# Kernel optimization log

Measured on AMD Instinct MI355X. Metric: run time of the kernel, lower is better.

The kernel has to match this reference:

```python
import jax, jax.numpy as jnp
import numpy as np

L, H, D_MODEL, FFN = 2, 8, 1024, 4096
HD = D_MODEL // H          # head size = 128
SCALE_BASE = 512           # XPOS scale_base
EPS = 1e-5                 # LayerNorm / GroupNorm eps (torch default)


def _layernorm(x, w, b):
    mu = x.mean(-1, keepdims=True)
    var = ((x - mu) ** 2).mean(-1, keepdims=True)
    return (x - mu) * jax.lax.rsqrt(var + EPS) * w + b


def _groupnorm(y, w, b):
    # GroupNorm(heads, v_dim) applied row-wise on (B*S, v_dim): normalize each head's HD slice.
    B, S, _ = y.shape
    yg = y.reshape(B, S, H, HD)
    mu = yg.mean(-1, keepdims=True)
    var = ((yg - mu) ** 2).mean(-1, keepdims=True)
    yn = ((yg - mu) * jax.lax.rsqrt(var + EPS)).reshape(B, S, H * HD)
    return yn * w + b


def _xpos_tables(S):
    # XPOS: scale = ((arange(0,HD,2)+0.4*HD)/(1.4*HD)) ** (pos/scale_base); sin/cos from fixed_pos_embedding(scale)
    scale_vec = (np.arange(0, HD, 2) + 0.4 * HD) / (1.4 * HD)            # (HD/2,)
    power = (np.arange(S, dtype=np.float64) / SCALE_BASE)[:, None]
    scale = scale_vec[None, :] ** power                                   # (S, HD/2)
    half = HD // 2
    inv_freq = 1.0 / (10000.0 ** (np.arange(half, dtype=np.float64) / half))
    ang = np.arange(S, dtype=np.float64)[:, None] * inv_freq[None, :]
    sin, cos = np.sin(ang), np.cos(ang)
    dup = lambda m: jnp.asarray(np.repeat(m, 2, axis=-1).astype(np.float32))  # duplicate_interleave -> (S, HD)
    return dup(sin * scale), dup(cos * scale), dup(sin / scale), dup(cos / scale)


def _rotate_every_two(x):
    x1, x2 = x[..., ::2], x[..., 1::2]
    return jnp.stack((-x2, x1), axis=-1).reshape(x.shape)


def _decay_mask(S):
    # gammas = 1 - exp(linspace(log(1/32), log(1/512), H)); D[h,n,m] = gamma_h^(n-m) * (n>=m)
    gammas = 1.0 - np.exp(np.linspace(np.log(1.0 / 32), np.log(1.0 / 512), H))
    n = np.arange(S)[:, None]
    m = np.arange(S)[None, :]
    diff = (n - m).astype(np.float64)
    D = np.where(n >= m, gammas[:, None, None] ** diff[None], 0.0)
    return jnp.asarray(D.astype(np.float32))  # (H, S, S)


def setup_inputs() -> dict:
    key = jax.random.key(0)
    ks = jax.random.split(key, 8)
    B, S = 2, 2048
    rn = lambda k, shape, s: jax.random.normal(k, shape, dtype=jnp.float32) * s
    return {
        "X": rn(ks[0], (B, S, D_MODEL), 1.0),
        "ln1_w": jnp.ones((L, D_MODEL), jnp.float32), "ln1_b": jnp.zeros((L, D_MODEL), jnp.float32),
        "ln2_w": jnp.ones((L, D_MODEL), jnp.float32), "ln2_b": jnp.zeros((L, D_MODEL), jnp.float32),
        "WQ": rn(ks[1], (L, H, D_MODEL, HD), 1.0 / D_MODEL),
        "WK": rn(ks[2], (L, H, D_MODEL, HD), 1.0 / D_MODEL),
        "WV": rn(ks[3], (L, H, D_MODEL, HD), 1.0 / D_MODEL),
        "gn_w": jnp.ones((L, D_MODEL), jnp.float32), "gn_b": jnp.zeros((L, D_MODEL), jnp.float32),
        "WG": rn(ks[4], (L, D_MODEL, D_MODEL), 1.0 / D_MODEL),
        "WO": rn(ks[5], (L, D_MODEL, D_MODEL), 1.0 / D_MODEL),
        "ffn_w1": rn(ks[6], (L, D_MODEL, FFN), 1.0 / np.sqrt(D_MODEL)),
        "ffn_b1": jnp.zeros((L, FFN), jnp.float32),
        "ffn_w2": rn(ks[7], (L, FFN, D_MODEL), 1.0 / np.sqrt(FFN)),
        "ffn_b2": jnp.zeros((L, D_MODEL), jnp.float32),
    }


def reference(X, ln1_w, ln1_b, ln2_w, ln2_b, WQ, WK, WV, gn_w, gn_b, WG, WO,
              ffn_w1, ffn_b1, ffn_w2, ffn_b2):
    B, S, _ = X.shape
    sinq, cosq, sink, cosk = _xpos_tables(S)   # (S, HD) each; K uses downscale (1/scale)
    Dm = _decay_mask(S)                         # (H, S, S)
    for i in range(L):
        Xn = _layernorm(X, ln1_w[i], ln1_b[i])
        Q = jnp.einsum('bsd,hdk->bhsk', Xn, WQ[i])
        K = jnp.einsum('bsd,hdk->bhsk', Xn, WK[i])
        V = jnp.einsum('bsd,hdk->bhsk', Xn, WV[i])
        Q = Q * cosq + _rotate_every_two(Q) * sinq
        K = K * cosk + _rotate_every_two(K) * sink
        scores = jnp.einsum('bhsk,bhtk->bhst', Q, K) * Dm[None]  # decay-masked retention
        Yh = jnp.einsum('bhst,bhtk->bhsk', scores, V)
        Y = Yh.transpose(0, 2, 1, 3).reshape(B, S, H * HD)        # concat heads
        Y = _groupnorm(Y, gn_w[i], gn_b[i])
        G = jax.nn.silu(Xn @ WG[i])                               # swish gate on layernormed input
        Y = (G * Y) @ WO[i] + X                                   # retention + residual
        Yn = _layernorm(Y, ln2_w[i], ln2_b[i])
        X = jax.nn.silu(Yn @ ffn_w1[i] + ffn_b1[i]) @ ffn_w2[i] + ffn_b2[i] + Y
    return X
```

## Files before the change

kernel.cpp:

```cpp
#include <hip/hip_runtime.h>
#include <cstdint>
#include <cstddef>

#define LN_ 2
#define HH 8
#define DM 1024
#define FFN_ 4096
#define HDD 128
#define SS 2048
#define BB 2
#define RR (BB*SS)

typedef __bf16 bf16x8 __attribute__((ext_vector_type(8)));
typedef __bf16 bf16x4 __attribute__((ext_vector_type(4)));
typedef __bf16 bf16x2 __attribute__((ext_vector_type(2)));
typedef float  f32x4  __attribute__((ext_vector_type(4)));

__device__ __forceinline__ float silu_f(float x) { return x / (1.0f + expf(-x)); }

__device__ __forceinline__ void glds16(const void* g, void* l) {
  __builtin_amdgcn_global_load_lds(
      (const __attribute__((address_space(1))) unsigned int*)g,
      (__attribute__((address_space(3))) unsigned int*)l, 16, 0, 0);
}


__device__ __forceinline__ int xcd_swz(int lin, int nblk) {
  return (lin & 7) * (nblk >> 3) + (lin >> 3);
}

__global__ void init_tables_k(float* __restrict__ sq, float* __restrict__ cq,
                              float* __restrict__ sk, float* __restrict__ ck,
                              float* __restrict__ lg2g) {
  int s = blockIdx.x, k = threadIdx.x;
  int j = k >> 1;
  double sv    = (2.0 * j + 0.4 * HDD) / (1.4 * HDD);
  double p     = (double)s / 512.0;
  double scale = pow(sv, p);
  double invf  = pow(10000.0, -((double)j) / 64.0);
  double ang   = (double)s * invf;
  double sn = sin(ang), cs = cos(ang);
  size_t idx = (size_t)s * HDD + k;
  sq[idx] = (float)(sn * scale);
  cq[idx] = (float)(cs * scale);
  sk[idx] = (float)(sn / scale);
  ck[idx] = (float)(cs / scale);
  if (s == 0 && k < HH) {
    double a0 = log(1.0 / 32.0), a1 = log(1.0 / 512.0);
    double x = a0 + (a1 - a0) * ((double)k / 7.0);
    lg2g[k] = (float)(log(1.0 - exp(x)) / log(2.0));
  }
}

__global__ __launch_bounds__(256) void ln_pack_k(
    const float* __restrict__ X, const float* __restrict__ w,
    const float* __restrict__ b, char* __restrict__ ph, char* __restrict__ pl) {
  const int row = blockIdx.x, tid = threadIdx.x;
  const float* x = X + (size_t)row * DM;
  float4 v = *(const float4*)(x + tid * 4);
  float s = v.x + v.y + v.z + v.w;
  float q = v.x * v.x + v.y * v.y + v.z * v.z + v.w * v.w;
#pragma unroll
  for (int o = 32; o > 0; o >>= 1) { s += __shfl_xor(s, o); q += __shfl_xor(q, o); }
  __shared__ float ss[4], qq[4];
  if ((tid & 63) == 0) { ss[tid >> 6] = s; qq[tid >> 6] = q; }
  __syncthreads();
  float S  = ss[0] + ss[1] + ss[2] + ss[3];
  float Qs = qq[0] + qq[1] + qq[2] + qq[3];
  float mu  = S * (1.0f / DM);
  float var = Qs * (1.0f / DM) - mu * mu;
  float rs  = 1.0f / sqrtf(var + 1e-5f);
  float4 wv = *(const float4*)(w + tid * 4);
  float4 bv = *(const float4*)(b + tid * 4);
  float y[4];
  y[0] = (v.x - mu) * rs * wv.x + bv.x;
  y[1] = (v.y - mu) * rs * wv.y + bv.y;
  y[2] = (v.z - mu) * rs * wv.z + bv.z;
  y[3] = (v.w - mu) * rs * wv.w + bv.w;
  bf16x4 hv, lv;
#pragma unroll
  for (int r = 0; r < 4; ++r) {
    __bf16 h = (__bf16)y[r];
    hv[r] = h;
    lv[r] = (__bf16)(y[r] - (float)h);
  }
  size_t tb = ((size_t)(row >> 7) * (DM / 64) + (tid >> 4)) * 16384;
  int off = (row & 127) * 128 + (((tid & 15) * 8) ^ ((row & 7) << 4));
  *(bf16x4*)(ph + tb + off) = hv;
  *(bf16x4*)(pl + tb + off) = lv;
}

__global__ __launch_bounds__(256) void packw_k(
    const float* __restrict__ W, char* __restrict__ dh, char* __restrict__ dl,
    int N, int qkv) {
  const int tn = blockIdx.x, tk = blockIdx.y, nkt = gridDim.y;
  __shared__ float L[64][132];
  const int k0 = tk * 64;
  const size_t srcbase = qkv ? ((size_t)tn * 131072 + (size_t)k0 * 128)
                             : ((size_t)k0 * N + (size_t)tn * 128);
  const int rstr = qkv ? 128 : N;
#pragma unroll
  for (int it = 0; it < 8; ++it) {
    int q = threadIdx.x + it * 256;
    int kk = q >> 5, c4 = (q & 31) * 4;
    float4 v = *(const float4*)(W + srcbase + (size_t)kk * rstr + c4);
    *(float4*)&L[kk][c4] = v;
  }
  __syncthreads();
  const size_t tb = ((size_t)tn * nkt + tk) * 16384;
#pragma unroll
  for (int it = 0; it < 4; ++it) {
    int o = threadIdx.x + it * 256;
    int n = o >> 3, k8 = o & 7;
    bf16x8 hv, lv;
#pragma unroll
    for (int j = 0; j < 8; ++j) {
      float x = L[k8 * 8 + j][n];
      __bf16 h = (__bf16)x;
      hv[j] = h;
      lv[j] = (__bf16)(x - (float)h);
    }
    int off = n * 128 + ((k8 * 16) ^ ((n & 7) << 4));
    *(bf16x8*)(dh + tb + off) = hv;
    *(bf16x8*)(dl + tb + off) = lv;
  }
}

__global__ __launch_bounds__(256) void vtpack_k(
    const float* __restrict__ V, char* __restrict__ dh, char* __restrict__ dl) {
  const int st = blockIdx.x, bh = blockIdx.y;
  __shared__ float L[64][132];
  const float* src = V + ((size_t)bh * SS + st * 64) * HDD;
#pragma unroll
  for (int it = 0; it < 8; ++it) {
    int q = threadIdx.x + it * 256;
    int r = q >> 5, c4 = (q & 31) * 4;
    *(float4*)&L[r][c4] = *(const float4*)(src + (size_t)r * HDD + c4);
  }
  __syncthreads();
  const size_t tb = ((size_t)bh * 32 + st) * 16384;
#pragma unroll
  for (int it = 0; it < 4; ++it) {
    int o = threadIdx.x + it * 256;
    int d = o >> 3, s8 = o & 7;
    bf16x8 hv, lv;
#pragma unroll
    for (int j = 0; j < 8; ++j) {
      float x = L[s8 * 8 + j][d];
      __bf16 h = (__bf16)x;
      hv[j] = h;
      lv[j] = (__bf16)(x - (float)h);
    }
    int off = d * 128 + ((s8 * 16) ^ ((d & 7) << 4));
    *(bf16x8*)(dh + tb + off) = hv;
    *(bf16x8*)(dl + tb + off) = lv;
  }
}

template <int NF>
__device__ __forceinline__ void gemm_main(
    const char* __restrict__ pAh, const char* __restrict__ pAl,
    const char* __restrict__ pBh, const char* __restrict__ pBl,
    size_t tA0, size_t tB0, int nkt, char* lds, f32x4 (&acc)[NF][4]) {
  const int tid = threadIdx.x, lane = tid & 63, w = tid >> 6;
  const int wm = w & 1, wn = w >> 1;
  const int swz = (lane & 7) << 4;
  const int l15 = lane & 15, l4 = lane >> 4;
  char* lAh = lds;
  char* lAl = lds + 16384;
  char* lBh = lds + 32768;
  char* lBl = lds + 32768 + NF * 4096;
  for (int t = 0; t < nkt; ++t) {
    const size_t oA = tA0 + (size_t)t * 16384;
    const size_t oB = tB0 + (size_t)t * 16384;
#pragma unroll
    for (int c = 0; c < 4; ++c) {
      const size_t go = (size_t)c * 4096 + w * 1024 + lane * 16;
      glds16(pAh + oA + go, lAh + c * 4096 + w * 1024);
      glds16(pAl + oA + go, lAl + c * 4096 + w * 1024);
    }
#pragma unroll
    for (int c = 0; c < NF; ++c) {
      const size_t go = (size_t)c * 4096 + w * 1024 + lane * 16;
      glds16(pBh + oB + go, lBh + c * 4096 + w * 1024);
      glds16(pBl + oB + go, lBl + c * 4096 + w * 1024);
    }
    __syncthreads();
#pragma unroll
    for (int ks = 0; ks < 2; ++ks) {
      const int kb = ks * 64 + l4 * 16;
      bf16x8 amh[4], aml[4], anh[NF], anl[NF];
#pragma unroll
      for (int f = 0; f < 4; ++f) {
        const int ra = (wm * 64 + f * 16 + l15) * 128 + (kb ^ swz);
        amh[f] = *(const bf16x8*)&lAh[ra];
        aml[f] = *(const bf16x8*)&lAl[ra];
      }
#pragma unroll
      for (int f = 0; f < NF; ++f) {
        const int rb = (wn * (NF * 16) + f * 16 + l15) * 128 + (kb ^ swz);
        anh[f] = *(const bf16x8*)&lBh[rb];
        anl[f] = *(const bf16x8*)&lBl[rb];
      }
#pragma unroll
      for (int nf = 0; nf < NF; ++nf)
#pragma unroll
        for (int mf = 0; mf < 4; ++mf) {
          acc[nf][mf] = __builtin_amdgcn_mfma_f32_16x16x32_bf16(
              anh[nf], amh[mf], acc[nf][mf], 0, 0, 0);
          acc[nf][mf] = __builtin_amdgcn_mfma_f32_16x16x32_bf16(
              anh[nf], aml[mf], acc[nf][mf], 0, 0, 0);
          acc[nf][mf] = __builtin_amdgcn_mfma_f32_16x16x32_bf16(
              anl[nf], amh[mf], acc[nf][mf], 0, 0, 0);
        }
    }
    __syncthreads();
  }
}

template <int MODE, int NF>
__global__ __launch_bounds__(256, (NF == 2 ? 3 : 2)) void mgemm_k(
    const char* __restrict__ pAh, const char* __restrict__ pAl,
    const char* __restrict__ pBh, const char* __restrict__ pBl,
    float* __restrict__ C, const float* __restrict__ bias,
    const float* __restrict__ resid, char* __restrict__ outH,
    char* __restrict__ outL, int N, int K) {
  __shared__ char lds[32768 + NF * 8192];
  const int lane = threadIdx.x & 63, w = threadIdx.x >> 6;
  const int wm = w & 1, wn = w >> 1;
  const int l15 = lane & 15, l4 = lane >> 4;
  const int lin = blockIdx.y * gridDim.x + blockIdx.x;
  const int swzb = xcd_swz(lin, gridDim.x * gridDim.y);
  const int bx = swzb % gridDim.x, by = swzb / gridDim.x;
  const int nkt = K >> 6;
  const size_t tA0 = (size_t)by * nkt * 16384;
  const size_t tB0 = (NF == 4) ? (size_t)bx * nkt * 16384
                               : (size_t)(bx >> 1) * nkt * 16384 + (size_t)(bx & 1) * 8192;
  f32x4 acc[NF][4];
#pragma unroll
  for (int i = 0; i < NF; ++i)
#pragma unroll
    for (int j = 0; j < 4; ++j) acc[i][j] = (f32x4){0.f, 0.f, 0.f, 0.f};

  gemm_main<NF>(pAh, pAl, pBh, pBl, tA0, tB0, nkt, lds, acc);

  const int mBase = by * 128 + wm * 64 + l15;
  const int nBase = bx * (NF * 32) + wn * (NF * 16) + l4 * 4;
#pragma unroll
  for (int nf = 0; nf < NF; ++nf)
#pragma unroll
    for (int mf = 0; mf < 4; ++mf) {
      const int m = mBase + mf * 16;
      const int n = nBase + nf * 16;
      f32x4 v = acc[nf][mf];
      if (MODE == 2) {
        f32x4 rz = *(const f32x4*)(resid + (size_t)m * N + n);
        v += rz;
        *(f32x4*)(C + (size_t)m * N + n) = v;
      } else if (MODE == 3) {
        f32x4 bz = *(const f32x4*)(bias + n);
        bf16x4 hv, lv;
#pragma unroll
        for (int r = 0; r < 4; ++r) {
          float y = silu_f(v[r] + bz[r]);
          __bf16 h = (__bf16)y;
          hv[r] = h;
          lv[r] = (__bf16)(y - (float)h);
        }
        size_t tb = ((size_t)(m >> 7) * (N >> 6) + (n >> 6)) * 16384;
        int off = (m & 127) * 128 + (((n & 63) * 2) ^ ((m & 7) << 4));
        *(bf16x4*)(outH + tb + off) = hv;
        *(bf16x4*)(outL + tb + off) = lv;
      } else {
        f32x4 bz = *(const f32x4*)(bias + n);
        f32x4 rz = *(const f32x4*)(resid + (size_t)m * N + n);
        v += bz + rz;
        *(f32x4*)(C + (size_t)m * N + n) = v;
      }
    }
}

__global__ __launch_bounds__(256, 2) void qkvg_k(
    const char* __restrict__ pXh, const char* __restrict__ pXl,
    const char* __restrict__ pWh, const char* __restrict__ pWl,
    float* __restrict__ V, float* __restrict__ G,
    char* __restrict__ pQh, char* __restrict__ pQl,
    char* __restrict__ pKh, char* __restrict__ pKl,
    const float* __restrict__ sq, const float* __restrict__ cq,
    const float* __restrict__ sk, const float* __restrict__ ck) {
  __shared__ char lds[65536];
  const int lane = threadIdx.x & 63, w = threadIdx.x >> 6;
  const int wm = w & 1, wn = w >> 1;
  const int l15 = lane & 15, l4 = lane >> 4;
  const int lin = ((blockIdx.z * 32) + blockIdx.y) * 8 + blockIdx.x;
  const int swzb = xcd_swz(lin, 1024);
  const int bx = swzb & 7, by = (swzb >> 3) & 31, z = swzb >> 8;
  const int nkt = DM >> 6;
  const size_t tA0 = (size_t)by * nkt * 16384;
  const size_t tB0 = (size_t)bx * nkt * 16384;
  const size_t wo = (size_t)z << 21;
  f32x4 acc[4][4];
#pragma unroll
  for (int i = 0; i < 4; ++i)
#pragma unroll
    for (int j = 0; j < 4; ++j) acc[i][j] = (f32x4){0.f, 0.f, 0.f, 0.f};

  gemm_main<4>(pXh, pXl, pWh + wo, pWl + wo, tA0, tB0, nkt, lds, acc);

  const int mBase = by * 128 + wm * 64 + l15;
  const int nBase = bx * 128 + wn * 64 + l4 * 4;
#pragma unroll
  for (int nf = 0; nf < 4; ++nf)
#pragma unroll
    for (int mf = 0; mf < 4; ++mf) {
      const int m = mBase + mf * 16;
      const int n = nBase + nf * 16;
      f32x4 v = acc[nf][mf];
      if (z == 2) {
        *(f32x4*)(V + (((size_t)(m >> 11) * HH + (n >> 7)) * SS + (m & (SS - 1)))
                          * HDD + (n & (HDD - 1))) = v;
      } else if (z == 3) {
#pragma unroll
        for (int r = 0; r < 4; ++r) v[r] = silu_f(v[r]);
        *(f32x4*)(G + (size_t)m * DM + n) = v;
      } else {
        const float* tsn = (z == 0) ? sq : sk;
        const float* tcs = (z == 0) ? cq : ck;
        char* oh = (z == 0) ? pQh : pKh;
        char* ol = (z == 0) ? pQl : pKl;
        int s = m & (SS - 1);
        int d = n & (HDD - 1);
        f32x4 sn = *(const f32x4*)(tsn + (size_t)s * HDD + d);
        f32x4 cn = *(const f32x4*)(tcs + (size_t)s * HDD + d);
        float o0 = v[0] * cn[0] - v[1] * sn[0];
        float o1 = v[1] * cn[1] + v[0] * sn[1];
        float o2 = v[2] * cn[2] - v[3] * sn[2];
        float o3 = v[3] * cn[3] + v[2] * sn[3];
        float oo[4] = {o0, o1, o2, o3};
        bf16x4 hv, lv;
#pragma unroll
        for (int r = 0; r < 4; ++r) {
          __bf16 h = (__bf16)oo[r];
          hv[r] = h;
          lv[r] = (__bf16)(oo[r] - (float)h);
        }
        size_t tile = ((size_t)(m >> 11) * HH + (n >> 7)) * 32 + (s >> 7) * 2 + (d >> 6);
        size_t off = tile * 16384 + (s & 127) * 128 + (((d & 63) * 2) ^ ((s & 7) << 4));
        *(bf16x4*)(oh + off) = hv;
        *(bf16x4*)(ol + off) = lv;
      }
    }
}

__global__ __launch_bounds__(256, 2) void mattn_k(
    const char* __restrict__ pQh, const char* __restrict__ pQl,
    const char* __restrict__ pKh, const char* __restrict__ pKl,
    const char* __restrict__ pVh, const char* __restrict__ pVl,
    const float* __restrict__ lg2g, float* __restrict__ Y) {
  __shared__ char Kls[2][2][8192];
  __shared__ char Vls[2][16384];
  __shared__ char Pls[2][8192];
  const int lin = blockIdx.y * 32 + blockIdx.x;
  const int swzb = xcd_swz(lin, 512);
  const int qt = 31 - (swzb & 31);
  const int bh = swzb >> 5;
  const int tid = threadIdx.x, lane = tid & 63, w = tid >> 6;
  const int wn = w & 1, wq = w >> 1;
  const int l15 = lane & 15, lg = lane >> 4;
  const float lg2 = lg2g[bh & 7];
  const size_t tb0 = (size_t)bh * 32;
  const int n0 = qt * 64;
  const int nt = qt + 1;

  bf16x8 qh[2][4], ql[2][4];
#pragma unroll
  for (int nf = 0; nf < 2; ++nf) {
    int rr = n0 + wn * 32 + nf * 16 + l15;
    size_t rowbase = (tb0 + (size_t)(rr >> 7) * 2) * 16384 + (size_t)(rr & 127) * 128;
    int sw = (rr & 7) << 4;
#pragma unroll
    for (int ks = 0; ks < 4; ++ks) {
      int d = ks * 32 + lg * 8;
      size_t a = rowbase + (size_t)(d >> 6) * 16384 + (((d & 63) * 2) ^ sw);
      qh[nf][ks] = *(const bf16x8*)(pQh + a);
      ql[nf][ks] = *(const bf16x8*)(pQl + a);
    }
  }

  f32x4 yacc[2][4];
#pragma unroll
  for (int i = 0; i < 2; ++i)
#pragma unroll
    for (int j = 0; j < 4; ++j) yacc[i][j] = (f32x4){0.f, 0.f, 0.f, 0.f};

  auto stageK = [&](int mt) {
    size_t half = (size_t)(mt & 1) * 8192;
#pragma unroll
    for (int dt = 0; dt < 2; ++dt) {
      size_t tile = (tb0 + (size_t)(mt >> 1) * 2 + dt) * 16384 + half;
#pragma unroll
      for (int c = 0; c < 2; ++c) {
        size_t go = (size_t)c * 4096 + w * 1024 + lane * 16;
        glds16(pKh + tile + go, &Kls[dt][0][c * 4096 + w * 1024]);
        glds16(pKl + tile + go, &Kls[dt][1][c * 4096 + w * 1024]);
      }
    }
  };
  auto stageV = [&](int mt) {
    size_t tile = (tb0 + mt) * 16384;
#pragma unroll
    for (int c = 0; c < 4; ++c) {
      size_t go = (size_t)c * 4096 + w * 1024 + lane * 16;
      glds16(pVh + tile + go, &Vls[0][c * 4096 + w * 1024]);
      glds16(pVl + tile + go, &Vls[1][c * 4096 + w * 1024]);
    }
  };

  stageK(0);
  stageV(0);
  __syncthreads();

  for (int mt = 0; mt < nt; ++mt) {
    f32x4 sacc[2][2];
#pragma unroll
    for (int i = 0; i < 2; ++i)
#pragma unroll
      for (int j = 0; j < 2; ++j) sacc[i][j] = (f32x4){0.f, 0.f, 0.f, 0.f};
#pragma unroll
    for (int ks = 0; ks < 4; ++ks) {
      int d = ks * 32 + lg * 8;
      bf16x8 kh[2], kl[2];
#pragma unroll
      for (int mf = 0; mf < 2; ++mf) {
        int m = wq * 32 + mf * 16 + l15;
        int off = (m & 63) * 128 + (((d & 63) * 2) ^ ((m & 7) << 4));
        kh[mf] = *(const bf16x8*)&Kls[d >> 6][0][off];
        kl[mf] = *(const bf16x8*)&Kls[d >> 6][1][off];
      }
#pragma unroll
      for (int nf = 0; nf < 2; ++nf)
#pragma unroll
        for (int mf = 0; mf < 2; ++mf) {
          sacc[nf][mf] = __builtin_amdgcn_mfma_f32_16x16x32_bf16(
              qh[nf][ks], kh[mf], sacc[nf][mf], 0, 0, 0);
          sacc[nf][mf] = __builtin_amdgcn_mfma_f32_16x16x32_bf16(
              qh[nf][ks], kl[mf], sacc[nf][mf], 0, 0, 0);
          sacc[nf][mf] = __builtin_amdgcn_mfma_f32_16x16x32_bf16(
              ql[nf][ks], kh[mf], sacc[nf][mf], 0, 0, 0);
        }
    }
    asm volatile("s_barrier" ::: "memory");
    if (mt + 1 < nt) stageK(mt + 1);

#pragma unroll
    for (int nf = 0; nf < 2; ++nf)
#pragma unroll
      for (int mf = 0; mf < 2; ++mf)
#pragma unroll
        for (int r = 0; r < 4; ++r) {
          int nl = wn * 32 + nf * 16 + lg * 4 + r;
          int ml = wq * 32 + mf * 16 + l15;
          int diff = (n0 + nl) - (mt * 64 + ml);
          float dec = (diff >= 0) ? exp2f((float)diff * lg2) : 0.0f;
          float p = sacc[nf][mf][r] * dec;
          __bf16 h = (__bf16)p;
          int off = nl * 128 + ((ml * 2) ^ ((nl & 7) << 4));
          *(__bf16*)&Pls[0][off] = h;
          *(__bf16*)&Pls[1][off] = (__bf16)(p - (float)h);
        }
    asm volatile("s_waitcnt lgkmcnt(0)" ::: "memory");
    asm volatile("s_barrier" ::: "memory");

#pragma unroll
    for (int ks = 0; ks < 2; ++ks) {
      int mchunk = ks * 32 + lg * 8;
      bf16x8 ph[2], pl2[2], vh[4], vl2[4];
#pragma unroll
      for (int nf = 0; nf < 2; ++nf) {
        int nl = wn * 32 + nf * 16 + l15;
        int off = nl * 128 + ((mchunk * 2) ^ ((nl & 7) << 4));
        ph[nf]  = *(const bf16x8*)&Pls[0][off];
        pl2[nf] = *(const bf16x8*)&Pls[1][off];
      }
#pragma unroll
      for (int df = 0; df < 4; ++df) {
        int d = wq * 64 + df * 16 + l15;
        int off = d * 128 + ((mchunk * 2) ^ ((d & 7) << 4));
        vh[df]  = *(const bf16x8*)&Vls[0][off];
        vl2[df] = *(const bf16x8*)&Vls[1][off];
      }
#pragma unroll
      for (int nf = 0; nf < 2; ++nf)
#pragma unroll
        for (int df = 0; df < 4; ++df) {
          yacc[nf][df] = __builtin_amdgcn_mfma_f32_16x16x32_bf16(
              ph[nf], vh[df], yacc[nf][df], 0, 0, 0);
          yacc[nf][df] = __builtin_amdgcn_mfma_f32_16x16x32_bf16(
              ph[nf], vl2[df], yacc[nf][df], 0, 0, 0);
          yacc[nf][df] = __builtin_amdgcn_mfma_f32_16x16x32_bf16(
              pl2[nf], vh[df], yacc[nf][df], 0, 0, 0);
        }
    }
    asm volatile("s_barrier" ::: "memory");
    if (mt + 1 < nt) stageV(mt + 1);
    __syncthreads();
  }

  const size_t yrow0 = (size_t)(bh >> 3) * SS + n0;
  const int hcol = (bh & 7) * HDD;
#pragma unroll
  for (int nf = 0; nf < 2; ++nf)
#pragma unroll
    for (int df = 0; df < 4; ++df)
#pragma unroll
      for (int r = 0; r < 4; ++r) {
        int nl = wn * 32 + nf * 16 + lg * 4 + r;
        int d  = wq * 64 + df * 16 + l15;
        Y[(yrow0 + nl) * DM + hcol + d] = yacc[nf][df][r];
      }
}

__global__ __launch_bounds__(256) void gn_gate_k(
    const float* __restrict__ Y, const float* __restrict__ w,
    const float* __restrict__ b, const float* __restrict__ G,
    char* __restrict__ ph, char* __restrict__ pl) {
  int g    = blockIdx.x * 4 + (threadIdx.x >> 6);
  int lane = threadIdx.x & 63;
  float2 v = *(const float2*)(Y + (size_t)g * HDD + lane * 2);
  float s = v.x + v.y, q = v.x * v.x + v.y * v.y;
#pragma unroll
  for (int o = 32; o > 0; o >>= 1) { s += __shfl_xor(s, o); q += __shfl_xor(q, o); }
  float mu  = s * (1.0f / HDD);
  float var = q * (1.0f / HDD) - mu * mu;
  float rs  = 1.0f / sqrtf(var + 1e-5f);
  int m   = g >> 3;
  int col = (g & 7) * HDD + lane * 2;
  float2 wv = *(const float2*)(w + col);
  float2 bv = *(const float2*)(b + col);
  float2 gv = *(const float2*)(G + (size_t)g * HDD + lane * 2);
  float ox = ((v.x - mu) * rs * wv.x + bv.x) * gv.x;
  float oy = ((v.y - mu) * rs * wv.y + bv.y) * gv.y;
  __bf16 hx = (__bf16)ox, hy = (__bf16)oy;
  bf16x2 hv, lv;
  hv[0] = hx; hv[1] = hy;
  lv[0] = (__bf16)(ox - (float)hx); lv[1] = (__bf16)(oy - (float)hy);
  size_t tb = ((size_t)(m >> 7) * (DM / 64) + (col >> 6)) * 16384;
  int off = (m & 127) * 128 + (((col & 63) * 2) ^ ((m & 7) << 4));
  *(bf16x2*)(ph + tb + off) = hv;
  *(bf16x2*)(pl + tb + off) = lv;
}

extern "C" void kernel_launch(void* const* d_in, const int* in_sizes, int n_in,
                              void* d_out, int out_size, void* d_ws, size_t ws_size,
                              hipStream_t stream) {
  (void)in_sizes; (void)n_in; (void)out_size; (void)ws_size;
  const float* X0   = (const float*)d_in[0];
  const float* ln1w = (const float*)d_in[1];
  const float* ln1b = (const float*)d_in[2];
  const float* ln2w = (const float*)d_in[3];
  const float* ln2b = (const float*)d_in[4];
  const float* WQ   = (const float*)d_in[5];
  const float* WK   = (const float*)d_in[6];
  const float* WV   = (const float*)d_in[7];
  const float* gnw  = (const float*)d_in[8];
  const float* gnb  = (const float*)d_in[9];
  const float* WG   = (const float*)d_in[10];
  const float* WO   = (const float*)d_in[11];
  const float* W1   = (const float*)d_in[12];
  const float* B1   = (const float*)d_in[13];
  const float* W2   = (const float*)d_in[14];
  const float* B2   = (const float*)d_in[15];

  char* wsb = (char*)d_ws;
  const size_t MB = 1 << 20;
  float* bufA = (float*)(wsb + 0 * MB);
  float* bufB = (float*)(wsb + 16 * MB);
  float* bufE = (float*)(wsb + 32 * MB);
  float* bufF = (float*)(wsb + 48 * MB);
  float* bufG = (float*)(wsb + 64 * MB);
  float* sq   = (float*)(wsb + 80 * MB);
  float* cq   = (float*)(wsb + 81 * MB);
  float* sk   = (float*)(wsb + 82 * MB);
  float* ck   = (float*)(wsb + 83 * MB);
  float* lg2g = (float*)(wsb + 84 * MB);
  char* pXh = wsb + 85 * MB;
  char* pXl = wsb + 93 * MB;
  char* pWh = wsb + 101 * MB;
  char* pWl = wsb + 127 * MB;
  char* R   = wsb + 153 * MB;
  char* pFh = R;
  char* pFl = R + 32 * MB;
  char* pQh = R;
  char* pQl = R + 8 * MB;
  char* pKh = R + 16 * MB;
  char* pKl = R + 24 * MB;
  char* pVh = R + 32 * MB;
  char* pVl = R + 40 * MB;
  const size_t oWQ = 0, oW1 = (size_t)10 << 20, oWO = (size_t)8 << 20,
               oW2 = (size_t)18 << 20;

  init_tables_k<<<SS, HDD, 0, stream>>>(sq, cq, sk, ck, lg2g);

  for (int i = 0; i < LN_; ++i) {
    const float* Xin = (i == 0) ? X0 : bufA;
    packw_k<<<dim3(8, 16), 256, 0, stream>>>(WQ + (size_t)i * 1048576, pWh + oWQ, pWl + oWQ, 1024, 1);
    packw_k<<<dim3(8, 16), 256, 0, stream>>>(WK + (size_t)i * 1048576, pWh + 2 * MB, pWl + 2 * MB, 1024, 1);
    packw_k<<<dim3(8, 16), 256, 0, stream>>>(WV + (size_t)i * 1048576, pWh + 4 * MB, pWl + 4 * MB, 1024, 1);
    packw_k<<<dim3(8, 16), 256, 0, stream>>>(WG + (size_t)i * 1048576, pWh + 6 * MB, pWl + 6 * MB, 1024, 0);
    packw_k<<<dim3(8, 16), 256, 0, stream>>>(WO + (size_t)i * 1048576, pWh + oWO, pWl + oWO, 1024, 0);
    packw_k<<<dim3(32, 16), 256, 0, stream>>>(W1 + (size_t)i * 4194304, pWh + oW1, pWl + oW1, 4096, 0);
    packw_k<<<dim3(8, 64), 256, 0, stream>>>(W2 + (size_t)i * 4194304, pWh + oW2, pWl + oW2, 1024, 0);

    ln_pack_k<<<RR, 256, 0, stream>>>(Xin, ln1w + i * DM, ln1b + i * DM, pXh, pXl);
    qkvg_k<<<dim3(8, 32, 4), 256, 0, stream>>>(pXh, pXl, pWh, pWl, bufE, bufF,
                                               pQh, pQl, pKh, pKl, sq, cq, sk, ck);
    vtpack_k<<<dim3(32, 16), 256, 0, stream>>>(bufE, pVh, pVl);
    mattn_k<<<dim3(32, 16), 256, 0, stream>>>(pQh, pQl, pKh, pKl, pVh, pVl, lg2g, bufG);
    gn_gate_k<<<RR * HH / 4, 256, 0, stream>>>(bufG, gnw + i * DM, gnb + i * DM,
                                               bufF, pXh, pXl);
    mgemm_k<2, 2><<<dim3(16, 32), 256, 0, stream>>>(pXh, pXl, pWh + oWO, pWl + oWO,
                                                    bufB, nullptr, Xin, nullptr, nullptr,
                                                    DM, DM);
    ln_pack_k<<<RR, 256, 0, stream>>>(bufB, ln2w + i * DM, ln2b + i * DM, pXh, pXl);
    mgemm_k<3, 4><<<dim3(32, 32), 256, 0, stream>>>(pXh, pXl, pWh + oW1, pWl + oW1,
                                                    nullptr, B1 + (size_t)i * FFN_,
                                                    nullptr, pFh, pFl, FFN_, DM);
    float* Xout = (i == LN_ - 1) ? (float*)d_out : bufA;
    mgemm_k<4, 2><<<dim3(16, 32), 256, 0, stream>>>(pFh, pFl, pWh + oW2, pWl + oW2,
                                                    Xout, B2 + (size_t)i * DM, bufB,
                                                    nullptr, nullptr, DM, FFN_);
  }
}
```

Baseline: 1.105 ms.

## Use 8-wave double-buffered GEMM mainloop for QKVG and FFN1 kernels

Adds a new 512-thread (8-wave) GEMM mainloop that double-buffers 128-wide K-steps in 128KB of LDS, issuing async global-to-LDS prefetches two tiles ahead and raising wave priority around the MFMA block. The QKVG projection and the FFN up-projection are switched to this mainloop with each wave owning a 64x32 output sub-tile, and the FFN1 epilogue moves into a dedicated kernel. The aim is to hide global load latency and raise MFMA utilisation through more waves and deeper prefetch. In exchange it uses much more LDS per block, which limits occupancy, and depends on hand-placed waitcnt and barrier ordering being correct.

```diff
diff --git a/kernel.cpp b/kernel.cpp
--- a/kernel.cpp
+++ b/kernel.cpp
@@ -218,13 +218,89 @@
   }
 }
 
+__device__ __forceinline__ void gemm8_main(
+    const char* __restrict__ pAh, const char* __restrict__ pAl,
+    const char* __restrict__ pBh, const char* __restrict__ pBl,
+    size_t tA0, size_t tB0, int nkt, char* lds, f32x4 (&acc)[2][4]) {
+  const int tid = threadIdx.x, lane = tid & 63, wid = tid >> 6;
+  const int wm = wid & 1, wn = wid >> 1;
+  const int l15 = lane & 15, l4 = lane >> 4;
+
+  auto stage = [&](int buf, int t) {
+    const size_t oA = tA0 + (size_t)t * 16384;
+    const size_t oB = tB0 + (size_t)t * 16384;
+    char* lb = lds + buf * 65536;
+#pragma unroll
+    for (int c = 0; c < 2; ++c) {
+      const size_t go = (size_t)c * 8192 + wid * 1024 + lane * 16;
+      const int lo = c * 8192 + wid * 1024;
+      glds16(pAh + oA + go, lb + lo);
+      glds16(pAl + oA + go, lb + 16384 + lo);
+      glds16(pBh + oB + go, lb + 32768 + lo);
+      glds16(pBl + oB + go, lb + 49152 + lo);
+    }
+  };
+
+  auto tile_comp = [&](int buf, bool pf, int pft) {
+    char* lb = lds + buf * 65536;
+    bf16x8 amh[2][4], aml[2][4], bnh[2][2], bnl[2][2];
+#pragma unroll
+    for (int ks = 0; ks < 2; ++ks) {
+      const int kb = ks * 64 + l4 * 16;
+#pragma unroll
+      for (int mf = 0; mf < 4; ++mf) {
+        const int rm = wm * 64 + mf * 16 + l15;
+        const int ra = rm * 128 + (kb ^ ((rm & 7) << 4));
+        amh[ks][mf] = *(const bf16x8*)(lb + ra);
+        aml[ks][mf] = *(const bf16x8*)(lb + 16384 + ra);
+      }
+#pragma unroll
+      for (int nf = 0; nf < 2; ++nf) {
+        const int rn = wn * 32 + nf * 16 + l15;
+        const int rb = rn * 128 + (kb ^ ((rn & 7) << 4));
+        bnh[ks][nf] = *(const bf16x8*)(lb + 32768 + rb);
+        bnl[ks][nf] = *(const bf16x8*)(lb + 49152 + rb);
+      }
+    }
+    asm volatile("s_waitcnt lgkmcnt(0)" ::: "memory");
+    asm volatile("s_barrier" ::: "memory");
+    if (pf) stage(buf, pft);
+    __builtin_amdgcn_s_setprio(1);
+#pragma unroll
+    for (int ks = 0; ks < 2; ++ks)
+#pragma unroll
+      for (int nf = 0; nf < 2; ++nf)
+#pragma unroll
+        for (int mf = 0; mf < 4; ++mf) {
+          acc[nf][mf] = __builtin_amdgcn_mfma_f32_16x16x32_bf16(
+              bnh[ks][nf], amh[ks][mf], acc[nf][mf], 0, 0, 0);
+          acc[nf][mf] = __builtin_amdgcn_mfma_f32_16x16x32_bf16(
+              bnh[ks][nf], aml[ks][mf], acc[nf][mf], 0, 0, 0);
+          acc[nf][mf] = __builtin_amdgcn_mfma_f32_16x16x32_bf16(
+              bnl[ks][nf], amh[ks][mf], acc[nf][mf], 0, 0, 0);
+        }
+    __builtin_amdgcn_s_setprio(0);
+  };
+
+  stage(0, 0);
+  asm volatile("" ::: "memory");
+  stage(1, 1);
+  for (int t = 0; t < nkt - 1; ++t) {
+    asm volatile("s_waitcnt vmcnt(8)" ::: "memory");
+    asm volatile("s_barrier" ::: "memory");
+    tile_comp(t & 1, t + 2 < nkt, t + 2);
+  }
+  asm volatile("s_waitcnt vmcnt(0)" ::: "memory");
+  asm volatile("s_barrier" ::: "memory");
+  tile_comp((nkt - 1) & 1, false, 0);
+}
+
 template <int MODE, int NF>
-__global__ __launch_bounds__(256, (NF == 2 ? 3 : 2)) void mgemm_k(
+__global__ __launch_bounds__(256, 3) void mgemm_k(
     const char* __restrict__ pAh, const char* __restrict__ pAl,
     const char* __restrict__ pBh, const char* __restrict__ pBl,
     float* __restrict__ C, const float* __restrict__ bias,
-    const float* __restrict__ resid, char* __restrict__ outH,
-    char* __restrict__ outL, int N, int K) {
+    const float* __restrict__ resid, int N, int K) {
   __shared__ char lds[32768 + NF * 8192];
   const int lane = threadIdx.x & 63, w = threadIdx.x >> 6;
   const int wm = w & 1, wn = w >> 1;
@@ -234,8 +310,7 @@
   const int bx = swzb % gridDim.x, by = swzb / gridDim.x;
   const int nkt = K >> 6;
   const size_t tA0 = (size_t)by * nkt * 16384;
-  const size_t tB0 = (NF == 4) ? (size_t)bx * nkt * 16384
-                               : (size_t)(bx >> 1) * nkt * 16384 + (size_t)(bx & 1) * 8192;
+  const size_t tB0 = (size_t)(bx >> 1) * nkt * 16384 + (size_t)(bx & 1) * 8192;
   f32x4 acc[NF][4];
 #pragma unroll
   for (int i = 0; i < NF; ++i)
@@ -257,20 +332,6 @@
         f32x4 rz = *(const f32x4*)(resid + (size_t)m * N + n);
         v += rz;
         *(f32x4*)(C + (size_t)m * N + n) = v;
-      } else if (MODE == 3) {
-        f32x4 bz = *(const f32x4*)(bias + n);
-        bf16x4 hv, lv;
-#pragma unroll
-        for (int r = 0; r < 4; ++r) {
-          float y = silu_f(v[r] + bz[r]);
-          __bf16 h = (__bf16)y;
-          hv[r] = h;
-          lv[r] = (__bf16)(y - (float)h);
-        }
-        size_t tb = ((size_t)(m >> 7) * (N >> 6) + (n >> 6)) * 16384;
-        int off = (m & 127) * 128 + (((n & 63) * 2) ^ ((m & 7) << 4));
-        *(bf16x4*)(outH + tb + off) = hv;
-        *(bf16x4*)(outL + tb + off) = lv;
       } else {
         f32x4 bz = *(const f32x4*)(bias + n);
         f32x4 rz = *(const f32x4*)(resid + (size_t)m * N + n);
@@ -280,7 +341,7 @@
     }
 }
 
-__global__ __launch_bounds__(256, 2) void qkvg_k(
+__global__ __launch_bounds__(512, 2) void qkvg8_k(
     const char* __restrict__ pXh, const char* __restrict__ pXl,
     const char* __restrict__ pWh, const char* __restrict__ pWl,
     float* __restrict__ V, float* __restrict__ G,
@@ -288,9 +349,9 @@
     char* __restrict__ pKh, char* __restrict__ pKl,
     const float* __restrict__ sq, const float* __restrict__ cq,
     const float* __restrict__ sk, const float* __restrict__ ck) {
-  __shared__ char lds[65536];
-  const int lane = threadIdx.x & 63, w = threadIdx.x >> 6;
-  const int wm = w & 1, wn = w >> 1;
+  __shared__ char lds[131072];
+  const int lane = threadIdx.x & 63, wid = threadIdx.x >> 6;
+  const int wm = wid & 1, wn = wid >> 1;
   const int l15 = lane & 15, l4 = lane >> 4;
   const int lin = ((blockIdx.z * 32) + blockIdx.y) * 8 + blockIdx.x;
   const int swzb = xcd_swz(lin, 1024);
@@ -299,18 +360,18 @@
   const size_t tA0 = (size_t)by * nkt * 16384;
   const size_t tB0 = (size_t)bx * nkt * 16384;
   const size_t wo = (size_t)z << 21;
-  f32x4 acc[4][4];
-#pragma unroll
-  for (int i = 0; i < 4; ++i)
+  f32x4 acc[2][4];
+#pragma unroll
+  for (int i = 0; i < 2; ++i)
 #pragma unroll
     for (int j = 0; j < 4; ++j) acc[i][j] = (f32x4){0.f, 0.f, 0.f, 0.f};
 
-  gemm_main<4>(pXh, pXl, pWh + wo, pWl + wo, tA0, tB0, nkt, lds, acc);
+  gemm8_main(pXh, pXl, pWh + wo, pWl + wo, tA0, tB0, nkt, lds, acc);
 
   const int mBase = by * 128 + wm * 64 + l15;
-  const int nBase = bx * 128 + wn * 64 + l4 * 4;
-#pragma unroll
-  for (int nf = 0; nf < 4; ++nf)
+  const int nBase = bx * 128 + wn * 32 + l4 * 4;
+#pragma unroll
+  for (int nf = 0; nf < 2; ++nf)
 #pragma unroll
     for (int mf = 0; mf < 4; ++mf) {
       const int m = mBase + mf * 16;
@@ -349,6 +410,55 @@
         *(bf16x4*)(oh + off) = hv;
         *(bf16x4*)(ol + off) = lv;
       }
+    }
+}
+
+__global__ __launch_bounds__(512, 2) void ffn1_8k(
+    const char* __restrict__ pAh, const char* __restrict__ pAl,
+    const char* __restrict__ pBh, const char* __restrict__ pBl,
+    const float* __restrict__ bias, char* __restrict__ outH,
+    char* __restrict__ outL) {
+  __shared__ char lds[131072];
+  const int lane = threadIdx.x & 63, wid = threadIdx.x >> 6;
+  const int wm = wid & 1, wn = wid >> 1;
+  const int l15 = lane & 15, l4 = lane >> 4;
+  const int lin = blockIdx.y * gridDim.x + blockIdx.x;
+  const int swzb = xcd_swz(lin, gridDim.x * gridDim.y);
+  const int bx = swzb % gridDim.x, by = swzb / gridDim.x;
+  const int nkt = DM >> 6;
+  const size_t tA0 = (size_t)by * nkt * 16384;
+  const size_t tB0 = (size_t)bx * nkt * 16384;
+  const int N = FFN_;
+  f32x4 acc[2][4];
+#pragma unroll
+  for (int i = 0; i < 2; ++i)
+#pragma unroll
+    for (int j = 0; j < 4; ++j) acc[i][j] = (f32x4){0.f, 0.f, 0.f, 0.f};
+
+  gemm8_main(pAh, pAl, pBh, pBl, tA0, tB0, nkt, lds, acc);
+
+  const int mBase = by * 128 + wm * 64 + l15;
+  const int nBase = bx * 128 + wn * 32 + l4 * 4;
+#pragma unroll
+  for (int nf = 0; nf < 2; ++nf)
+#pragma unroll
+    for (int mf = 0; mf < 4; ++mf) {
+      const int m = mBase + mf * 16;
+      const int n = nBase + nf * 16;
+      f32x4 v = acc[nf][mf];
+      f32x4 bz = *(const f32x4*)(bias + n);
+      bf16x4 hv, lv;
+#pragma unroll
+      for (int r = 0; r < 4; ++r) {
+        float y = silu_f(v[r] + bz[r]);
+        __bf16 h = (__bf16)y;
+        hv[r] = h;
+        lv[r] = (__bf16)(y - (float)h);
+      }
+      size_t tb = ((size_t)(m >> 7) * (N >> 6) + (n >> 6)) * 16384;
+      int off = (m & 127) * 128 + (((n & 63) * 2) ^ ((m & 7) << 4));
+      *(bf16x4*)(outH + tb + off) = hv;
+      *(bf16x4*)(outL + tb + off) = lv;
     }
 }
 
@@ -612,22 +722,20 @@
     packw_k<<<dim3(8, 64), 256, 0, stream>>>(W2 + (size_t)i * 4194304, pWh + oW2, pWl + oW2, 1024, 0);
 
     ln_pack_k<<<RR, 256, 0, stream>>>(Xin, ln1w + i * DM, ln1b + i * DM, pXh, pXl);
-    qkvg_k<<<dim3(8, 32, 4), 256, 0, stream>>>(pXh, pXl, pWh, pWl, bufE, bufF,
-                                               pQh, pQl, pKh, pKl, sq, cq, sk, ck);
+    qkvg8_k<<<dim3(8, 32, 4), 512, 0, stream>>>(pXh, pXl, pWh, pWl, bufE, bufF,
+                                                pQh, pQl, pKh, pKl, sq, cq, sk, ck);
     vtpack_k<<<dim3(32, 16), 256, 0, stream>>>(bufE, pVh, pVl);
     mattn_k<<<dim3(32, 16), 256, 0, stream>>>(pQh, pQl, pKh, pKl, pVh, pVl, lg2g, bufG);
     gn_gate_k<<<RR * HH / 4, 256, 0, stream>>>(bufG, gnw + i * DM, gnb + i * DM,
                                                bufF, pXh, pXl);
     mgemm_k<2, 2><<<dim3(16, 32), 256, 0, stream>>>(pXh, pXl, pWh + oWO, pWl + oWO,
-                                                    bufB, nullptr, Xin, nullptr, nullptr,
-                                                    DM, DM);
+                                                    bufB, nullptr, Xin, DM, DM);
     ln_pack_k<<<RR, 256, 0, stream>>>(bufB, ln2w + i * DM, ln2b + i * DM, pXh, pXl);
-    mgemm_k<3, 4><<<dim3(32, 32), 256, 0, stream>>>(pXh, pXl, pWh + oW1, pWl + oW1,
-                                                    nullptr, B1 + (size_t)i * FFN_,
-                                                    nullptr, pFh, pFl, FFN_, DM);
+    ffn1_8k<<<dim3(32, 32), 512, 0, stream>>>(pXh, pXl, pWh + oW1, pWl + oW1,
+                                              B1 + (size_t)i * FFN_, pFh, pFl);
     float* Xout = (i == LN_ - 1) ? (float*)d_out : bufA;
     mgemm_k<4, 2><<<dim3(16, 32), 256, 0, stream>>>(pFh, pFl, pWh + oW2, pWl + oW2,
                                                     Xout, B2 + (size_t)i * DM, bufB,
-                                                    nullptr, nullptr, DM, FFN_);
-  }
-}
+                                                    DM, FFN_);
+  }
+}
```

Result: slower. 1.194 ms (+8.0%).
